# Kernel optimization log

Hardware: AMD Instinct MI355X
Metric: run time of the kernel (lower is better)

Reference implementation:

```python
import jax, jax.numpy as jnp
import numpy as np

N_NODES = 100000
N_EDGES = 1200000
D_IN = 64
D_HID = 64


def _gcn_layer(h_in, W, b, src, dst, norm, n_nodes):
    # h_in: [N, d_in]; W: [d_in, d_out]; norm: [E_total] symmetric deg norm
    h = h_in @ W                                  # [N, d_out]
    msg = h[src] * norm[:, None]                  # gather + scale, [E_total, d_out]
    agg = jax.ops.segment_sum(msg, dst, num_segments=n_nodes)  # scatter-add
    return agg + b


def _prelu(x, a):
    # per-channel PReLU: a broadcasts over nodes
    return jnp.where(x >= 0, x, a * x)


def setup_inputs() -> dict:
    key = jax.random.key(0)
    ks = jax.random.split(key, 8)
    x = jax.random.normal(ks[0], (N_NODES, D_IN), dtype=jnp.float32)
    edge_index = jax.random.randint(ks[1], (2, N_EDGES), 0, N_NODES, dtype=jnp.int64)
    # Glorot-ish weights, PyG GCNConv defaults: weight + bias; PReLU init slope 0.25
    W1 = jax.random.normal(ks[2], (D_IN, D_HID), dtype=jnp.float32) / np.sqrt(D_IN)
    b1 = jnp.zeros((D_HID,), dtype=jnp.float32)
    a1 = jnp.full((D_HID,), 0.25, dtype=jnp.float32)
    W2 = jax.random.normal(ks[3], (D_HID, D_HID), dtype=jnp.float32) / np.sqrt(D_HID)
    b2 = jnp.zeros((D_HID,), dtype=jnp.float32)
    a2 = jnp.full((D_HID,), 0.25, dtype=jnp.float32)
    return {"x": x, "edge_index": edge_index, "W1": W1, "b1": b1, "a1": a1,
            "W2": W2, "b2": b2, "a2": a2}


def reference(x, edge_index, W1, b1, a1, W2, b2, a2):
    n = x.shape[0]
    # add self-loops (GCNConv default add_self_loops=True)
    loops = jnp.arange(n, dtype=edge_index.dtype)
    src = jnp.concatenate([edge_index[0], loops])
    dst = jnp.concatenate([edge_index[1], loops])
    # symmetric normalization: deg computed on destination with unit edge weights
    deg = jax.ops.segment_sum(jnp.ones_like(src, dtype=x.dtype), dst, num_segments=n)
    dinv = jnp.where(deg > 0, jax.lax.rsqrt(deg), 0.0)
    norm = dinv[src] * dinv[dst]                  # [E + N]

    h = _gcn_layer(x, W1, b1, src, dst, norm, n)
    h = _prelu(h, a1)
    h = _gcn_layer(h, W2, b2, src, dst, norm, n)
    h = _prelu(h, a2)
    return h
```

## Files before the change

### kernel.cpp

```cpp
#include <hip/hip_runtime.h>
#include <hip/hip_bf16.h>
#include <hip/hip_fp16.h>

#define D 64
#define NB 256
#define BSHIFT 8
#define NBK 512
#define SUBS 8
#define SCAP 1024
#define CHUNK 8192
#define AGN 32
#define BFSTRIDE 16

typedef _Float16 f16x8 __attribute__((ext_vector_type(8)));
typedef float    f32x4 __attribute__((ext_vector_type(4)));


__global__ void __launch_bounds__(256, 4)
k_bin_gemm(const int* __restrict__ src, const int* __restrict__ dst,
           unsigned* __restrict__ records, int* __restrict__ bucket_fill,
           int E, int nbin,
           const float* __restrict__ X, const float* __restrict__ W,
           __half* __restrict__ H, int n, int ntiles, int gemmb) {
    __shared__ int cnt[NBK];
    __shared__ int gbase[NBK];
    const int t = threadIdx.x;

    if ((int)blockIdx.x < nbin) {
        const int slot = blockIdx.x & (SUBS - 1);
        cnt[t] = 0; cnt[t + 256] = 0;
        __syncthreads();

        const int base_e = blockIdx.x * CHUNK;
        unsigned rec[32];
        unsigned br[32];
#pragma unroll
        for (int i = 0; i < 8; ++i) {
            const int e0 = base_e + i * 1024 + t * 4;
            if (e0 + 3 < E) {
                int4 s4 = *reinterpret_cast<const int4*>(src + e0);
                int4 d4 = *reinterpret_cast<const int4*>(dst + e0);
                int ss[4] = {s4.x, s4.y, s4.z, s4.w};
                int dd[4] = {d4.x, d4.y, d4.z, d4.w};
#pragma unroll
                for (int j = 0; j < 4; ++j) {
                    int bk = dd[j] >> BSHIFT;
                    rec[i * 4 + j] = ((unsigned)ss[j] << BSHIFT) | (unsigned)(dd[j] & (NB - 1));
                    int rank = atomicAdd(&cnt[bk], 1);
                    br[i * 4 + j] = ((unsigned)bk << 16) | (unsigned)rank;
                }
            } else {
#pragma unroll
                for (int j = 0; j < 4; ++j) {
                    int e = e0 + j;
                    if (e < E) {
                        int s = src[e], d = dst[e];
                        int bk = d >> BSHIFT;
                        rec[i * 4 + j] = ((unsigned)s << BSHIFT) | (unsigned)(d & (NB - 1));
                        int rank = atomicAdd(&cnt[bk], 1);
                        br[i * 4 + j] = ((unsigned)bk << 16) | (unsigned)rank;
                    } else {
                        br[i * 4 + j] = 0xFFFFFFFFu;
                    }
                }
            }
        }
        __syncthreads();
#pragma unroll
        for (int rep = 0; rep < NBK / 256; ++rep) {
            int bk = t + rep * 256;
            if (cnt[bk] > 0)
                gbase[bk] = atomicAdd(&bucket_fill[(bk * SUBS + slot) * BFSTRIDE], cnt[bk]);
        }
        __syncthreads();
#pragma unroll
        for (int i = 0; i < 32; ++i) {
            if (br[i] != 0xFFFFFFFFu) {
                int bk = br[i] >> 16;
                int idx = gbase[bk] + (int)(br[i] & 0xFFFF);
                if (idx < SCAP)
                    records[((size_t)bk * SUBS + slot) * SCAP + idx] = rec[i];
            }
        }
    } else {
        const int lane = t & 63;
        const int wv   = t >> 6;
        const int r16  = lane & 15;
        const int g4   = lane >> 4;

        f16x8 Bh[4][2], Bl[4][2];
#pragma unroll
        for (int ct = 0; ct < 4; ++ct)
#pragma unroll
            for (int kt = 0; kt < 2; ++kt)
#pragma unroll
                for (int j = 0; j < 8; ++j) {
                    float w = W[(kt * 32 + g4 * 8 + j) * D + ct * 16 + r16];
                    _Float16 h = (_Float16)w;
                    Bh[ct][kt][j] = h;
                    Bl[ct][kt][j] = (_Float16)(w - (float)h);
                }

        const int gw = (blockIdx.x - nbin) * 4 + wv;
        for (int tile = gw; tile < ntiles; tile += gemmb * 4) {
            const int nb16 = tile * 16;
            int row = nb16 + r16;
            if (row > n - 1) row = n - 1;
            const float* xp = X + (size_t)row * D + g4 * 8;
            float4 x0 = *reinterpret_cast<const float4*>(xp);
            float4 x1 = *reinterpret_cast<const float4*>(xp + 4);
            float4 x2 = *reinterpret_cast<const float4*>(xp + 32);
            float4 x3 = *reinterpret_cast<const float4*>(xp + 36);
            float xs[16] = {x0.x, x0.y, x0.z, x0.w, x1.x, x1.y, x1.z, x1.w,
                            x2.x, x2.y, x2.z, x2.w, x3.x, x3.y, x3.z, x3.w};
            f16x8 Ah[2], Al[2];
#pragma unroll
            for (int kt = 0; kt < 2; ++kt)
#pragma unroll
                for (int j = 0; j < 8; ++j) {
                    float v = xs[kt * 8 + j];
                    _Float16 h = (_Float16)v;
                    Ah[kt][j] = h;
                    Al[kt][j] = (_Float16)(v - (float)h);
                }

            f32x4 acc[4];
#pragma unroll
            for (int ct = 0; ct < 4; ++ct)
                acc[ct] = (f32x4){0.f, 0.f, 0.f, 0.f};
#pragma unroll
            for (int ct = 0; ct < 4; ++ct) {
#pragma unroll
                for (int kt = 0; kt < 2; ++kt) {
                    acc[ct] = __builtin_amdgcn_mfma_f32_16x16x32_f16(Ah[kt], Bh[ct][kt], acc[ct], 0, 0, 0);
                    acc[ct] = __builtin_amdgcn_mfma_f32_16x16x32_f16(Al[kt], Bh[ct][kt], acc[ct], 0, 0, 0);
                    acc[ct] = __builtin_amdgcn_mfma_f32_16x16x32_f16(Ah[kt], Bl[ct][kt], acc[ct], 0, 0, 0);
                }
            }
#pragma unroll
            for (int ct = 0; ct < 4; ++ct)
#pragma unroll
                for (int r = 0; r < 4; ++r) {
                    int node = nb16 + g4 * 4 + r;
                    if (node < n)
                        H[(size_t)node * D + ct * 16 + r16] = __float2half_rn(acc[ct][r]);
                }
        }
    }
}


__global__ void k_csr(const unsigned* __restrict__ records,
                      const int* __restrict__ bucket_fill,
                      int* __restrict__ edge_base,
                      int* __restrict__ rowbeg, int* __restrict__ rowcnt,
                      float* __restrict__ dinv,
                      int* __restrict__ csr_src, int n) {
    __shared__ int cnt[NB];
    __shared__ int excl[NB];
    __shared__ int wsum[4];
    __shared__ int sbase;
    __shared__ int stage[SUBS * SCAP];

    const int t = threadIdx.x;
    const int b = blockIdx.x;
    const int lane = t & 63;

    int subcnt[SUBS];
    int cnt_e = 0;
#pragma unroll
    for (int s = 0; s < SUBS; ++s) {
        subcnt[s] = bucket_fill[(b * SUBS + s) * BFSTRIDE];
        cnt_e += subcnt[s];
    }

    cnt[t] = 0;
    __syncthreads();
#pragma unroll
    for (int s = 0; s < SUBS; ++s) {
        const size_t so = ((size_t)b * SUBS + s) * SCAP;
        for (int i = t; i < subcnt[s]; i += 256)
            atomicAdd(&cnt[records[so + i] & (NB - 1)], 1);
    }
    __syncthreads();

    const int c0 = cnt[t];
    int v = c0;
#pragma unroll
    for (int off = 1; off < 64; off <<= 1) {
        int u = __shfl_up(v, off, 64);
        if (lane >= off) v += u;
    }
    if (lane == 63) wsum[t >> 6] = v;
    if (t == 0) sbase = atomicAdd(edge_base, cnt_e);
    __syncthreads();
    int pre = 0;
#pragma unroll
    for (int w = 0; w < 4; ++w)
        if (w < (t >> 6)) pre += wsum[w];
    const int ex = v + pre - c0;
    excl[t] = ex;
    const int base = sbase;
    {
        int node = b * NB + t;
        if (node < n) {
            rowbeg[node] = base + ex;
            rowcnt[node] = c0;
            dinv[node]   = rsqrtf((float)(c0 + 1));
        }
    }
    cnt[t] = 0;
    __syncthreads();

#pragma unroll
    for (int s = 0; s < SUBS; ++s) {
        const size_t so = ((size_t)b * SUBS + s) * SCAP;
        for (int i = t; i < subcnt[s]; i += 256) {
            unsigned r = records[so + i];
            int d8 = r & (NB - 1);
            int rank = atomicAdd(&cnt[d8], 1);
            stage[excl[d8] + rank] = (int)(r >> BSHIFT);
        }
    }
    __syncthreads();

    for (int i = t; i < cnt_e; i += 256)
        csr_src[base + i] = stage[i];
}

__device__ __forceinline__ void edge_accum(const __half* __restrict__ Hn,
                                           const int* __restrict__ csr_src,
                                           int beg, int end, int part, float acc[8]) {
    int idx[8];
#pragma unroll
    for (int j = 0; j < 8; ++j)
        idx[j] = (beg + j < end) ? csr_src[beg + j] : 0;
    int k = beg;
    while (k < end) {
        int s[8];
        float w[8];
#pragma unroll
        for (int j = 0; j < 8; ++j) {
            s[j] = idx[j];
            w[j] = (k + j < end) ? 1.f : 0.f;
        }
        int kn = k + 8;
#pragma unroll
        for (int j = 0; j < 8; ++j)
            idx[j] = (kn + j < end) ? csr_src[kn + j] : 0;
        uint4 g[8];
#pragma unroll
        for (int j = 0; j < 8; ++j)
            g[j] = *reinterpret_cast<const uint4*>(Hn + (size_t)s[j] * D + part);
#pragma unroll
        for (int j = 0; j < 8; ++j) {
            const __half2* p = reinterpret_cast<const __half2*>(&g[j]);
#pragma unroll
            for (int i = 0; i < 4; ++i) {
                float2 f = __half22float2(p[i]);
                acc[2 * i + 0] += w[j] * f.x;
                acc[2 * i + 1] += w[j] * f.y;
            }
        }
        k = kn;
    }
}

__device__ __forceinline__ void edge_accum_sc(const __half* __restrict__ Hn,
                                              const int* __restrict__ csr_src,
                                              const float* __restrict__ dinv,
                                              int beg, int end, int part, float acc[8]) {
    int idx[8];
#pragma unroll
    for (int j = 0; j < 8; ++j)
        idx[j] = (beg + j < end) ? csr_src[beg + j] : 0;
    int k = beg;
    while (k < end) {
        int s[8];
        float w[8];
#pragma unroll
        for (int j = 0; j < 8; ++j) {
            s[j] = idx[j];
            w[j] = (k + j < end) ? dinv[s[j]] : 0.f;
        }
        int kn = k + 8;
#pragma unroll
        for (int j = 0; j < 8; ++j)
            idx[j] = (kn + j < end) ? csr_src[kn + j] : 0;
        uint4 g[8];
#pragma unroll
        for (int j = 0; j < 8; ++j)
            g[j] = *reinterpret_cast<const uint4*>(Hn + (size_t)s[j] * D + part);
#pragma unroll
        for (int j = 0; j < 8; ++j) {
            const __half2* p = reinterpret_cast<const __half2*>(&g[j]);
#pragma unroll
            for (int i = 0; i < 4; ++i) {
                float2 f = __half22float2(p[i]);
                acc[2 * i + 0] += w[j] * f.x;
                acc[2 * i + 1] += w[j] * f.y;
            }
        }
        k = kn;
    }
}


__global__ void __launch_bounds__(256, 4)
k_agg_gemm(const __half* __restrict__ Hn1,
           const int* __restrict__ rowbeg,
           const int* __restrict__ rowcnt,
           const int* __restrict__ csr_src,
           const float* __restrict__ dinv,
           const float* __restrict__ b1, const float* __restrict__ a1,
           const float* __restrict__ W2,
           __half* __restrict__ Hn2, int n) {
    __shared__ float Yl[AGN][68];
    __shared__ float Zl[AGN][68];

    const int t    = threadIdx.x;
    const int lane = t & 63;
    const int wv   = t >> 6;
    const int r16  = lane & 15;
    const int g4   = lane >> 4;
    const int rt   = wv >> 1;
    const int cp   = wv & 1;

    f16x8 Bh[2][2], Bl[2][2];
#pragma unroll
    for (int ci = 0; ci < 2; ++ci)
#pragma unroll
        for (int kt = 0; kt < 2; ++kt)
#pragma unroll
            for (int j = 0; j < 8; ++j) {
                float w = W2[(kt * 32 + g4 * 8 + j) * D + (cp * 2 + ci) * 16 + r16];
                _Float16 h = (_Float16)w;
                Bh[ci][kt][j] = h;
                Bl[ci][kt][j] = (_Float16)(w - (float)h);
            }

    const int nl   = t >> 3;
    const int part = (t & 7) * 8;
    const int node = blockIdx.x * AGN + nl;

    if (node < n) {
        float di = dinv[node];
        float acc[8];
        {
            uint4 g = *reinterpret_cast<const uint4*>(Hn1 + (size_t)node * D + part);
            const __half2* p = reinterpret_cast<const __half2*>(&g);
#pragma unroll
            for (int i = 0; i < 4; ++i) {
                float2 f = __half22float2(p[i]);
                acc[2 * i + 0] = f.x * di;
                acc[2 * i + 1] = f.y * di;
            }
        }
        const int beg = rowbeg[node];
        edge_accum_sc(Hn1, csr_src, dinv, beg, beg + rowcnt[node], part, acc);

        const float4 b0 = *reinterpret_cast<const float4*>(b1 + part);
        const float4 b4 = *reinterpret_cast<const float4*>(b1 + part + 4);
        const float4 a0 = *reinterpret_cast<const float4*>(a1 + part);
        const float4 a4 = *reinterpret_cast<const float4*>(a1 + part + 4);
        float y0 = acc[0] * di + b0.x, y1 = acc[1] * di + b0.y;
        float y2 = acc[2] * di + b0.z, y3 = acc[3] * di + b0.w;
        float y4 = acc[4] * di + b4.x, y5 = acc[5] * di + b4.y;
        float y6 = acc[6] * di + b4.z, y7 = acc[7] * di + b4.w;
        Yl[nl][part + 0] = (y0 >= 0.f) ? y0 : a0.x * y0;
        Yl[nl][part + 1] = (y1 >= 0.f) ? y1 : a0.y * y1;
        Yl[nl][part + 2] = (y2 >= 0.f) ? y2 : a0.z * y2;
        Yl[nl][part + 3] = (y3 >= 0.f) ? y3 : a0.w * y3;
        Yl[nl][part + 4] = (y4 >= 0.f) ? y4 : a4.x * y4;
        Yl[nl][part + 5] = (y5 >= 0.f) ? y5 : a4.y * y5;
        Yl[nl][part + 6] = (y6 >= 0.f) ? y6 : a4.z * y6;
        Yl[nl][part + 7] = (y7 >= 0.f) ? y7 : a4.w * y7;
        if ((t & 7) == 0) Yl[nl][64] = di;
    }
    __syncthreads();

    {
        f32x4 acc2[2];
        acc2[0] = (f32x4){0.f, 0.f, 0.f, 0.f};
        acc2[1] = (f32x4){0.f, 0.f, 0.f, 0.f};
#pragma unroll
        for (int kt = 0; kt < 2; ++kt) {
            const float* yp = &Yl[rt * 16 + r16][kt * 32 + g4 * 8];
            f16x8 Ah, Al;
#pragma unroll
            for (int j = 0; j < 8; ++j) {
                float v = yp[j];
                _Float16 h = (_Float16)v;
                Ah[j] = h;
                Al[j] = (_Float16)(v - (float)h);
            }
#pragma unroll
            for (int ci = 0; ci < 2; ++ci) {
                acc2[ci] = __builtin_amdgcn_mfma_f32_16x16x32_f16(Ah, Bh[ci][kt], acc2[ci], 0, 0, 0);
                acc2[ci] = __builtin_amdgcn_mfma_f32_16x16x32_f16(Al, Bh[ci][kt], acc2[ci], 0, 0, 0);
                acc2[ci] = __builtin_amdgcn_mfma_f32_16x16x32_f16(Ah, Bl[ci][kt], acc2[ci], 0, 0, 0);
            }
        }
#pragma unroll
        for (int ci = 0; ci < 2; ++ci)
#pragma unroll
            for (int r = 0; r < 4; ++r) {
                int row = rt * 16 + g4 * 4 + r;
                float dr = Yl[row][64];
                Zl[row][(cp * 2 + ci) * 16 + r16] = acc2[ci][r] * dr;
            }
    }
    __syncthreads();

    if (node >= n) return;
    float4 z0 = *reinterpret_cast<const float4*>(&Zl[nl][part]);
    float4 z1 = *reinterpret_cast<const float4*>(&Zl[nl][part + 4]);
    __half2 h0 = __floats2half2_rn(z0.x, z0.y);
    __half2 h1 = __floats2half2_rn(z0.z, z0.w);
    __half2 h2 = __floats2half2_rn(z1.x, z1.y);
    __half2 h3 = __floats2half2_rn(z1.z, z1.w);
    uint4 pack;
    pack.x = *reinterpret_cast<unsigned int*>(&h0);
    pack.y = *reinterpret_cast<unsigned int*>(&h1);
    pack.z = *reinterpret_cast<unsigned int*>(&h2);
    pack.w = *reinterpret_cast<unsigned int*>(&h3);
    *reinterpret_cast<uint4*>(Hn2 + (size_t)node * D + part) = pack;
}


__global__ void k_aggregate(const __half* __restrict__ Hn,
                            const int* __restrict__ rowbeg,
                            const int* __restrict__ rowcnt,
                            const int* __restrict__ csr_src,
                            const float* __restrict__ dinv,
                            const float* __restrict__ b, const float* __restrict__ a,
                            float* __restrict__ out, int n) {
    int t = blockIdx.x * blockDim.x + threadIdx.x;
    int node = t >> 3;
    if (node >= n) return;
    int part = (t & 7) * 8;

    float di = dinv[node];
    float acc[8];
    {
        uint4 g = *reinterpret_cast<const uint4*>(Hn + (size_t)node * D + part);
        const __half2* p = reinterpret_cast<const __half2*>(&g);
#pragma unroll
        for (int i = 0; i < 4; ++i) {
            float2 f = __half22float2(p[i]);
            acc[2 * i + 0] = f.x;
            acc[2 * i + 1] = f.y;
        }
    }
    const int beg = rowbeg[node];
    edge_accum(Hn, csr_src, beg, beg + rowcnt[node], part, acc);

    const float4 b0 = *reinterpret_cast<const float4*>(b + part);
    const float4 b4 = *reinterpret_cast<const float4*>(b + part + 4);
    const float4 a0 = *reinterpret_cast<const float4*>(a + part);
    const float4 a4 = *reinterpret_cast<const float4*>(a + part + 4);
    float4 r0, r1;
    r0.x = acc[0] * di + b0.x; r0.y = acc[1] * di + b0.y;
    r0.z = acc[2] * di + b0.z; r0.w = acc[3] * di + b0.w;
    r1.x = acc[4] * di + b4.x; r1.y = acc[5] * di + b4.y;
    r1.z = acc[6] * di + b4.z; r1.w = acc[7] * di + b4.w;
    r0.x = (r0.x >= 0.f) ? r0.x : a0.x * r0.x;
    r0.y = (r0.y >= 0.f) ? r0.y : a0.y * r0.y;
    r0.z = (r0.z >= 0.f) ? r0.z : a0.z * r0.z;
    r0.w = (r0.w >= 0.f) ? r0.w : a0.w * r0.w;
    r1.x = (r1.x >= 0.f) ? r1.x : a4.x * r1.x;
    r1.y = (r1.y >= 0.f) ? r1.y : a4.y * r1.y;
    r1.z = (r1.z >= 0.f) ? r1.z : a4.z * r1.z;
    r1.w = (r1.w >= 0.f) ? r1.w : a4.w * r1.w;
    float* o = out + (size_t)node * D + part;
    *reinterpret_cast<float4*>(o) = r0;
    *reinterpret_cast<float4*>(o + 4) = r1;
}

extern "C" void kernel_launch(void* const* d_in, const int* in_sizes, int n_in,
                              void* d_out, int out_size, void* d_ws, size_t ws_size,
                              hipStream_t stream) {
    const float* x  = (const float*)d_in[0];
    const int*   ei = (const int*)  d_in[1];
    const float* W1 = (const float*)d_in[2];
    const float* b1 = (const float*)d_in[3];
    const float* a1 = (const float*)d_in[4];
    const float* W2 = (const float*)d_in[5];
    const float* b2 = (const float*)d_in[6];
    const float* a2 = (const float*)d_in[7];
    float* out = (float*)d_out;

    const int n   = in_sizes[0] / D;
    const int E   = in_sizes[1] / 2;
    const int n64 = n * D;

    const int* src = ei;
    const int* dst = ei + E;

    const int nbuckets = (n + NB - 1) >> BSHIFT;

    int*      bucket_fill = (int*)d_ws;
    int*      edge_base   = bucket_fill + 60000;
    unsigned* records     = (unsigned*)(bucket_fill + 4096 * BFSTRIDE);
    int*      rowbeg      = (int*)(records + (size_t)nbuckets * SUBS * SCAP);
    int*      rowcnt      = rowbeg + ((n + 256) & ~255);
    float*    dinv        = (float*)(rowcnt + ((n + 256) & ~255));
    int*      csr_src     = (int*)(dinv + ((n + 256) & ~255));
    __half*   Hn1         = (__half*)(csr_src + ((E + 255) & ~255));
    __half*   Hn2         = Hn1 + (((size_t)n64 + 256) & ~(size_t)255);

    const int B = 256;
    const int nbin   = (E + CHUNK - 1) / CHUNK;
    const int gemmb  = 877;
    const int ntiles = (n + 15) / 16;

    hipMemsetAsync(bucket_fill, 0, 4096 * BFSTRIDE * sizeof(int), stream);

    k_bin_gemm<<<nbin + gemmb, B, 0, stream>>>(src, dst, records, bucket_fill, E, nbin,
                                               x, W1, Hn1, n, ntiles, gemmb);
    k_csr<<<nbuckets, B, 0, stream>>>(records, bucket_fill, edge_base,
                                      rowbeg, rowcnt, dinv, csr_src, n);
    k_agg_gemm<<<(n + AGN - 1) / AGN, B, 0, stream>>>(Hn1, rowbeg, rowcnt, csr_src, dinv,
                                                      b1, a1, W2, Hn2, n);
    k_aggregate<<<(n * 8 + B - 1) / B, B, 0, stream>>>(Hn2, rowbeg, rowcnt, csr_src, dinv,
                                                       b2, a2, out, n);
}
```

Baseline: 178.5 us.

## Stage W2 split-fp16 in shared memory, drop Z staging, prefetch dinv

The fused aggregate+GEMM kernel now builds the hi/lo fp16 split of W2 once per block in shared memory in MFMA-friendly layout, rather than holding B fragments in registers. It also writes the MFMA outputs straight to global memory as scalar halves, which removes the Zl buffer and a barrier. Occupancy is raised to 5 blocks per SIMD. Separately, the edge loop in the self-contained accumulate helper now loads dinv for the next batch of neighbours one iteration ahead. The cost is extra LDS traffic per block and uncoalesced 2-byte stores in place of 16-byte packed stores.

```diff
diff --git a/kernel.cpp b/kernel.cpp
--- a/kernel.cpp
+++ b/kernel.cpp
@@ -271,9 +271,13 @@
                                               const float* __restrict__ dinv,
                                               int beg, int end, int part, float acc[8]) {
     int idx[8];
+    float dv[8];
 #pragma unroll
     for (int j = 0; j < 8; ++j)
         idx[j] = (beg + j < end) ? csr_src[beg + j] : 0;
+#pragma unroll
+    for (int j = 0; j < 8; ++j)
+        dv[j] = dinv[idx[j]];
     int k = beg;
     while (k < end) {
         int s[8];
@@ -281,12 +285,15 @@
 #pragma unroll
         for (int j = 0; j < 8; ++j) {
             s[j] = idx[j];
-            w[j] = (k + j < end) ? dinv[s[j]] : 0.f;
+            w[j] = (k + j < end) ? dv[j] : 0.f;
         }
         int kn = k + 8;
 #pragma unroll
         for (int j = 0; j < 8; ++j)
             idx[j] = (kn + j < end) ? csr_src[kn + j] : 0;
+#pragma unroll
+        for (int j = 0; j < 8; ++j)
+            dv[j] = dinv[idx[j]];
         uint4 g[8];
 #pragma unroll
         for (int j = 0; j < 8; ++j)
@@ -306,7 +313,7 @@
 }
 
 
-__global__ void __launch_bounds__(256, 4)
+__global__ void __launch_bounds__(256, 5)
 k_agg_gemm(const __half* __restrict__ Hn1,
            const int* __restrict__ rowbeg,
            const int* __restrict__ rowcnt,
@@ -315,29 +322,27 @@
            const float* __restrict__ b1, const float* __restrict__ a1,
            const float* __restrict__ W2,
            __half* __restrict__ Hn2, int n) {
+    __shared__ _Float16 W2h[D * D];
+    __shared__ _Float16 W2s[D * D];
     __shared__ float Yl[AGN][68];
-    __shared__ float Zl[AGN][68];
-
-    const int t    = threadIdx.x;
-    const int lane = t & 63;
-    const int wv   = t >> 6;
-    const int r16  = lane & 15;
-    const int g4   = lane >> 4;
-    const int rt   = wv >> 1;
-    const int cp   = wv & 1;
-
-    f16x8 Bh[2][2], Bl[2][2];
-#pragma unroll
-    for (int ci = 0; ci < 2; ++ci)
-#pragma unroll
-        for (int kt = 0; kt < 2; ++kt)
-#pragma unroll
-            for (int j = 0; j < 8; ++j) {
-                float w = W2[(kt * 32 + g4 * 8 + j) * D + (cp * 2 + ci) * 16 + r16];
-                _Float16 h = (_Float16)w;
-                Bh[ci][kt][j] = h;
-                Bl[ci][kt][j] = (_Float16)(w - (float)h);
-            }
+
+    const int t = threadIdx.x;
+
+#pragma unroll
+    for (int q = 0; q < 4; ++q) {
+        float4 wq = *reinterpret_cast<const float4*>(W2 + t * 16 + q * 4);
+        float ws[4] = {wq.x, wq.y, wq.z, wq.w};
+#pragma unroll
+        for (int m = 0; m < 4; ++m) {
+            int widx = t * 16 + q * 4 + m;
+            int k   = widx >> 6;
+            int col = widx & 63;
+            int li  = (((k >> 5) * 4 + ((k >> 3) & 3)) * 64 + col) * 8 + (k & 7);
+            _Float16 h = (_Float16)ws[m];
+            W2h[li] = h;
+            W2s[li] = (_Float16)(ws[m] - (float)h);
+        }
+    }
 
     const int nl   = t >> 3;
     const int part = (t & 7) * 8;
@@ -380,6 +385,13 @@
     __syncthreads();
 
     {
+        const int lane = t & 63;
+        const int wvq  = t >> 6;
+        const int r16  = lane & 15;
+        const int g4   = lane >> 4;
+        const int rt   = wvq >> 1;
+        const int cp   = wvq & 1;
+
         f32x4 acc2[2];
         acc2[0] = (f32x4){0.f, 0.f, 0.f, 0.f};
         acc2[1] = (f32x4){0.f, 0.f, 0.f, 0.f};
@@ -396,9 +408,12 @@
             }
 #pragma unroll
             for (int ci = 0; ci < 2; ++ci) {
-                acc2[ci] = __builtin_amdgcn_mfma_f32_16x16x32_f16(Ah, Bh[ci][kt], acc2[ci], 0, 0, 0);
-                acc2[ci] = __builtin_amdgcn_mfma_f32_16x16x32_f16(Al, Bh[ci][kt], acc2[ci], 0, 0, 0);
-                acc2[ci] = __builtin_amdgcn_mfma_f32_16x16x32_f16(Ah, Bl[ci][kt], acc2[ci], 0, 0, 0);
+                int li = ((kt * 4 + g4) * 64 + (cp * 2 + ci) * 16 + r16) * 8;
+                f16x8 Bh = *reinterpret_cast<const f16x8*>(&W2h[li]);
+                f16x8 Bl = *reinterpret_cast<const f16x8*>(&W2s[li]);
+                acc2[ci] = __builtin_amdgcn_mfma_f32_16x16x32_f16(Ah, Bh, acc2[ci], 0, 0, 0);
+                acc2[ci] = __builtin_amdgcn_mfma_f32_16x16x32_f16(Al, Bh, acc2[ci], 0, 0, 0);
+                acc2[ci] = __builtin_amdgcn_mfma_f32_16x16x32_f16(Ah, Bl, acc2[ci], 0, 0, 0);
             }
         }
 #pragma unroll
@@ -406,25 +421,14 @@
 #pragma unroll
             for (int r = 0; r < 4; ++r) {
                 int row = rt * 16 + g4 * 4 + r;
-                float dr = Yl[row][64];
-                Zl[row][(cp * 2 + ci) * 16 + r16] = acc2[ci][r] * dr;
-            }
-    }
-    __syncthreads();
-
-    if (node >= n) return;
-    float4 z0 = *reinterpret_cast<const float4*>(&Zl[nl][part]);
-    float4 z1 = *reinterpret_cast<const float4*>(&Zl[nl][part + 4]);
-    __half2 h0 = __floats2half2_rn(z0.x, z0.y);
-    __half2 h1 = __floats2half2_rn(z0.z, z0.w);
-    __half2 h2 = __floats2half2_rn(z1.x, z1.y);
-    __half2 h3 = __floats2half2_rn(z1.z, z1.w);
-    uint4 pack;
-    pack.x = *reinterpret_cast<unsigned int*>(&h0);
-    pack.y = *reinterpret_cast<unsigned int*>(&h1);
-    pack.z = *reinterpret_cast<unsigned int*>(&h2);
-    pack.w = *reinterpret_cast<unsigned int*>(&h3);
-    *reinterpret_cast<uint4*>(Hn2 + (size_t)node * D + part) = pack;
+                int nd  = blockIdx.x * AGN + row;
+                if (nd < n) {
+                    float dr = Yl[row][64];
+                    Hn2[(size_t)nd * D + (cp * 2 + ci) * 16 + r16] =
+                        __float2half_rn(acc2[ci][r] * dr);
+                }
+            }
+    }
 }
 
 
```

New measurement: 175.9 us. Within noise of the previous version (-1.5%).
